# Performance work log

Hardware: AMD Instinct MI355X
Metric: run time of the kernel (lower is better)

The kernel has to match this reference:

```python
import jax, jax.numpy as jnp
import numpy as np

H, KVH, D, HID = 32, 8, 128, 4096
ROPE_LEN, THETA = 8192, 10000.0
MASK_OUT, MIN_REMAIN = 0.9, 128


def _rope_tables(dtype):
    inv_freq = 1.0 / (THETA ** (jnp.arange(0, D, 2, dtype=jnp.float32) / D))
    freqs = jnp.arange(ROPE_LEN, dtype=jnp.float32)[:, None] * inv_freq[None, :]
    emb = jnp.concatenate([freqs, freqs], axis=-1)  # [8192, 128]
    return jnp.cos(emb).astype(dtype), jnp.sin(emb).astype(dtype)


def _rotate_half(x):
    x1, x2 = x[..., : D // 2], x[..., D // 2:]
    return jnp.concatenate([-x2, x1], axis=-1)


def _apply_rope(x, pos, cos, sin):
    c, s = cos[pos][None, None], sin[pos][None, None]  # [1,1,L,D]
    return x * c + _rotate_half(x) * s


def setup_inputs() -> dict:
    key = jax.random.key(0)
    ks = jax.random.split(key, 11)
    S = 4096
    f = jnp.float32
    return {
        "hidden_states": jax.random.normal(ks[0], (1, 1, HID), f),
        "key_cache": jax.random.normal(ks[1], (1, H, S, D), f),
        "val_cache": jax.random.normal(ks[2], (1, H, S, D), f),
        "Wq": jax.random.normal(ks[3], (HID, HID), f) * 0.02,
        "Wk": jax.random.normal(ks[4], (HID, KVH * D), f) * 0.02,
        "Wv": jax.random.normal(ks[5], (HID, KVH * D), f) * 0.02,
        "Wo": jax.random.normal(ks[6], (HID, HID), f) * 0.02,
        "hash_proj1": jax.random.normal(ks[7], (1, H, D, D), f) * 0.001,
        "hash_bias1": jnp.zeros((1, H, 1, D), f),
        "hash_proj2": jax.random.normal(ks[8], (1, H, D, D), f) * 0.001,
        "hash_bias2": jnp.zeros((1, H, 1, D), f),
    }


def reference(hidden_states, key_cache, val_cache, Wq, Wk, Wv, Wo,
              hash_proj1, hash_bias1, hash_proj2, hash_bias2):
    B, Q, _ = hidden_states.shape  # B=1, Q=1 (decode step)
    G = H // KVH
    dtype = hidden_states.dtype

    # projections -> [B, heads, Q, D]
    ques = (hidden_states @ Wq).reshape(B, Q, H, D).transpose(0, 2, 1, 3)
    k_new = (hidden_states @ Wk).reshape(B, Q, KVH, D).transpose(0, 2, 1, 3)
    v_new = (hidden_states @ Wv).reshape(B, Q, KVH, D).transpose(0, 2, 1, 3)
    k_new = jnp.repeat(k_new, G, axis=1)  # repeat_kv
    v_new = jnp.repeat(v_new, G, axis=1)

    keys = jnp.concatenate([key_cache, k_new], axis=2)  # [1,H,K,D]
    vals = jnp.concatenate([val_cache, v_new], axis=2)
    K = keys.shape[2]

    cos, sin = _rope_tables(dtype)
    q_pos = K - Q + jnp.arange(Q)
    k_pos = jnp.arange(K)
    q_r = _apply_rope(ques, q_pos, cos, sin)
    k_r = _apply_rope(keys, k_pos, cos, sin)

    # per-head hash MLP: silu layer with residue, then linear layer with residue
    def hash_fn(x):
        h = jax.nn.silu(jnp.einsum('bhld,bhde->bhle', x, hash_proj1) + hash_bias1) + x
        h = (jnp.einsum('bhld,bhde->bhle', h, hash_proj2) + hash_bias2) + h
        return h

    q_hash = jnp.sign(hash_fn(q_r))
    k_hash = jnp.sign(hash_fn(k_r))
    draft_score = jnp.einsum('bhqd,bhkd->bhqk', q_hash, k_hash)  # LSH similarity

    num_remain = max(min(K, MIN_REMAIN), K - int(K * MASK_OUT))
    _, idx = jax.lax.top_k(draft_score, num_remain)  # [B,H,Q,num_remain]

    neg = jnp.finfo(dtype).min
    mask = jnp.full((B, H, Q, K), neg, dtype=dtype)
    bi = jnp.arange(B)[:, None, None, None]
    hi = jnp.arange(H)[None, :, None, None]
    qi = jnp.arange(Q)[None, None, :, None]
    mask = mask.at[bi, hi, qi, idx].set(0.0)

    scores = jnp.einsum('bhqd,bhkd->bhqk', q_r, k_r) / np.sqrt(D) + mask
    attn = jax.nn.softmax(scores, axis=-1)
    out = jnp.einsum('bhqk,bhkd->bhqd', attn, vals)
    out = out.transpose(0, 2, 1, 3).reshape(B, Q, HID) @ Wo
    return out
```

## Files before the change

### kernel.cpp

```cpp
#include <hip/hip_runtime.h>
#include <math.h>

#define NH 32
#define NKVH 8
#define HD 128

typedef _Float16 half8 __attribute__((ext_vector_type(8)));
typedef float f32x4 __attribute__((ext_vector_type(4)));

#define OFF_QPROJ 0
#define OFF_KNEW  4096
#define OFF_VNEW  5120
#define OFF_QR    6144
#define OFF_QHASH 10240
#define OFF_TAB   10368

__global__ void init_kernel(float* __restrict__ ws, float* __restrict__ out, int K) {
    int idx = blockIdx.x * 256 + threadIdx.x;
    if (idx < K * 64) {
        int pos = idx >> 6, d = idx & 63;
        double inv = exp(-((double)d / 64.0) * log(10000.0));
        double ang = (double)pos * inv;
        double s, c;
        sincos(ang, &s, &c);
        ws[OFF_TAB + idx]                  = (float)c;
        ws[OFF_TAB + (size_t)K * 64 + idx] = (float)s;
    }
    if (idx < 6144) ws[OFF_QPROJ + idx] = 0.f;
    if (idx < 4096) out[idx] = 0.f;
    size_t off_attn = OFF_TAB + 2 * (size_t)K * 64 + 2 * (size_t)NH * K;
    if (idx < 4096) ws[off_attn + idx] = 0.f;
}

__global__ __launch_bounds__(256) void pt16_prep(const float* __restrict__ hp1,
        const float* __restrict__ hp2, float* __restrict__ ws, int K) {
    const int tg  = blockIdx.x * 256 + threadIdx.x;
    const int h   = blockIdx.y >> 1, mat = blockIdx.y & 1;
    const int lane = tg & 63, nt = (tg >> 6) & 7, ks = tg >> 9;
    const int kbase = ks * 32 + ((tg >> 4) & 3) * 8;
    const int n = nt * 16 + (tg & 15);
    const float* P = (mat ? hp2 : hp1) + (size_t)h * 16384;
    half8 v;
#pragma unroll
    for (int j = 0; j < 8; ++j) v[j] = (_Float16)P[(size_t)(kbase + j) * 128 + n];
    size_t off_pt = OFF_TAB + 2 * (size_t)K * 64 + 2 * (size_t)NH * K + 4096 + 2 * (size_t)NH * 512;
    ((half8*)(ws + off_pt))[(size_t)(h * 2 + mat) * 2048 + tg] = v;
}

__global__ __launch_bounds__(256) void qkv_gemv(const float* __restrict__ hidden,
        const float* __restrict__ Wq, const float* __restrict__ Wk,
        const float* __restrict__ Wv, float* __restrict__ ws) {
    __shared__ float hs[32];
    const int tid = threadIdx.x;
    const int col = (blockIdx.x * 256 + tid) * 4;
    const int i0  = blockIdx.y * 32;
    if (tid < 32) hs[tid] = hidden[i0 + tid];
    __syncthreads();
    const float* W; int ld, wcol;
    if (col < 4096)      { W = Wq; ld = 4096; wcol = col; }
    else if (col < 5120) { W = Wk; ld = 1024; wcol = col - 4096; }
    else                 { W = Wv; ld = 1024; wcol = col - 5120; }
    const float* p = W + (size_t)i0 * ld + wcol;
    float4 acc = {0.f, 0.f, 0.f, 0.f};
#pragma unroll 4
    for (int ii = 0; ii < 32; ++ii) {
        float4 w4 = *(const float4*)p;
        float hh = hs[ii];
        acc.x = fmaf(hh, w4.x, acc.x); acc.y = fmaf(hh, w4.y, acc.y);
        acc.z = fmaf(hh, w4.z, acc.z); acc.w = fmaf(hh, w4.w, acc.w);
        p += ld;
    }
    atomicAdd(&ws[OFF_QPROJ + col + 0], acc.x);
    atomicAdd(&ws[OFF_QPROJ + col + 1], acc.y);
    atomicAdd(&ws[OFF_QPROJ + col + 2], acc.z);
    atomicAdd(&ws[OFF_QPROJ + col + 3], acc.w);
}

__global__ __launch_bounds__(128) void qhash_kernel(const float* __restrict__ hp1,
        const float* __restrict__ hb1, const float* __restrict__ hp2,
        const float* __restrict__ hb2, float* __restrict__ ws, int S) {
    const int h = blockIdx.x, d = threadIdx.x;
    const int K = S + 1;
    __shared__ float X[128], H1[128];
    float q  = ws[OFF_QPROJ + h * 128 + d];
    float qp = ws[OFF_QPROJ + h * 128 + (d ^ 64)];
    const float* cosT = ws + OFF_TAB;
    const float* sinT = cosT + (size_t)K * 64;
    float cs = cosT[(size_t)S * 64 + (d & 63)];
    float sn = sinT[(size_t)S * 64 + (d & 63)];
    float r = (d < 64) ? -qp : qp;
    float qr = q * cs + r * sn;
    X[d] = qr;
    ws[OFF_QR + h * 128 + d] = qr;
    __syncthreads();
    const float* P1 = hp1 + (size_t)h * 16384;
    float t = hb1[h * 128 + d];
    for (int i = 0; i < 128; ++i) t = fmaf(X[i], P1[i * 128 + d], t);
    float u = t / (1.f + expf(-t)) + X[d];
    H1[d] = u;
    __syncthreads();
    const float* P2 = hp2 + (size_t)h * 16384;
    float t2 = hb2[h * 128 + d] + u;
    for (int i = 0; i < 128; ++i) t2 = fmaf(H1[i], P2[i * 128 + d], t2);
    unsigned long long bal = __ballot(t2 > 0.f);
    if ((d & 63) == 0)
        ((unsigned long long*)(ws + OFF_QHASH))[h * 2 + (d >> 6)] = bal;
}

__global__ __launch_bounds__(256, 2) void key_kernel(const float* __restrict__ key_cache,
        const float* __restrict__ hb1, const float* __restrict__ hb2,
        float* __restrict__ ws, int S) {
    const int K  = S + 1;
    const int h  = blockIdx.y;
    const int k0 = blockIdx.x * 64;
    const int tid = threadIdx.x;
    const int wv = tid >> 6, lane = tid & 63;

    __shared__ float    XF[64 * 132];
    __shared__ _Float16 XH[64 * 136];
    __shared__ _Float16 BST[2 * 4096];
    __shared__ unsigned short HB[64 * 8];
    __shared__ float    QV[128];

    const float* cosT = ws + OFF_TAB;
    const float* sinT = cosT + (size_t)K * 64;
    float* scores = ws + OFF_TAB + 2 * (size_t)K * 64;
    int*   draft  = (int*)(scores + (size_t)NH * K);
    size_t off_pt = OFF_TAB + 2 * (size_t)K * 64 + 2 * (size_t)NH * K + 4096 + 2 * (size_t)NH * 512;
    const _Float16* PT1 = (const _Float16*)(ws + off_pt) + (size_t)(h * 2 + 0) * 16384;
    const _Float16* PT2 = (const _Float16*)(ws + off_pt) + (size_t)(h * 2 + 1) * 16384;

    if (tid < 128) QV[tid] = ws[OFF_QR + h * 128 + tid];

    const int key = tid >> 2, qq = tid & 3, d0 = qq * 16;
    const int kg = k0 + key;
    float lo[16], hi[16];
    if (kg < K) {
        const float* row = (kg < S) ? key_cache + ((size_t)h * S + kg) * 128
                                    : ws + OFF_KNEW + (h >> 2) * 128;
#pragma unroll
        for (int i4 = 0; i4 < 4; ++i4) {
            float4 xa = *(const float4*)(row + d0 + i4 * 4);
            float4 xb = *(const float4*)(row + 64 + d0 + i4 * 4);
            float4 cc = *(const float4*)(cosT + (size_t)kg * 64 + d0 + i4 * 4);
            float4 ss = *(const float4*)(sinT + (size_t)kg * 64 + d0 + i4 * 4);
            lo[i4*4+0] = xa.x * cc.x - xb.x * ss.x;  hi[i4*4+0] = xb.x * cc.x + xa.x * ss.x;
            lo[i4*4+1] = xa.y * cc.y - xb.y * ss.y;  hi[i4*4+1] = xb.y * cc.y + xa.y * ss.y;
            lo[i4*4+2] = xa.z * cc.z - xb.z * ss.z;  hi[i4*4+2] = xb.z * cc.z + xa.z * ss.z;
            lo[i4*4+3] = xa.w * cc.w - xb.w * ss.w;  hi[i4*4+3] = xb.w * cc.w + xa.w * ss.w;
        }
    } else {
#pragma unroll
        for (int i = 0; i < 16; ++i) { lo[i] = 0.f; hi[i] = 0.f; }
    }
#pragma unroll
    for (int i = 0; i < 16; ++i) {
        XF[key * 132 + d0 + i]      = lo[i];
        XF[key * 132 + 64 + d0 + i] = hi[i];
        XH[key * 136 + d0 + i]      = (_Float16)lo[i];
        XH[key * 136 + 64 + d0 + i] = (_Float16)hi[i];
    }
    __syncthreads();

    {
        float part = 0.f;
#pragma unroll
        for (int i = 0; i < 16; ++i)
            part = fmaf(QV[d0 + i], lo[i], fmaf(QV[64 + d0 + i], hi[i], part));
        part += __shfl_xor(part, 1);
        part += __shfl_xor(part, 2);
        if (qq == 0 && kg < K) scores[(size_t)h * K + kg] = part * 0.08838834764831845f;
    }

    float b1v[8], b2v[8];
#pragma unroll
    for (int nt = 0; nt < 8; ++nt) {
        b1v[nt] = hb1[h * 128 + nt * 16 + (lane & 15)];
        b2v[nt] = hb2[h * 128 + nt * 16 + (lane & 15)];
    }

    f32x4 acc[8];
    const int m = lane & 15, quad = lane >> 4;

#define GEMM_MFMA(PT)                                                              \
    {                                                                              \
        _Pragma("unroll") for (int nt = 0; nt < 8; ++nt)                           \
            acc[nt] = (f32x4){0.f, 0.f, 0.f, 0.f};                                 \
        const half8* src = (const half8*)(PT);                                     \
        half8 pre0 = src[tid * 2], pre1 = src[tid * 2 + 1];                        \
        for (int c = 0; c < 4; ++c) {                                              \
            half8* dst = (half8*)&BST[(c & 1) * 4096];                             \
            dst[tid * 2] = pre0; dst[tid * 2 + 1] = pre1;                          \
            __syncthreads();                                                       \
            if (c < 3) {                                                           \
                pre0 = src[(c + 1) * 512 + tid * 2];                               \
                pre1 = src[(c + 1) * 512 + tid * 2 + 1];                           \
            }                                                                      \
            half8 afrag = *(const half8*)&XH[(wv * 16 + m) * 136 + c * 32 + quad * 8]; \
            _Pragma("unroll") for (int nt = 0; nt < 8; ++nt) {                     \
                half8 bfrag = *(const half8*)&BST[(c & 1) * 4096 + nt * 512 + lane * 8]; \
                acc[nt] = __builtin_amdgcn_mfma_f32_16x16x32_f16(afrag, bfrag, acc[nt], 0, 0, 0); \
            }                                                                      \
        }                                                                          \
    }

    GEMM_MFMA(PT1)
#pragma unroll
    for (int nt = 0; nt < 8; ++nt) {
        const int n = nt * 16 + m;
#pragma unroll
        for (int r = 0; r < 4; ++r) {
            const int kk = wv * 16 + quad * 4 + r;
            float t = acc[nt][r] + b1v[nt];
            float x = XF[kk * 132 + n];
            float h1v = t / (1.f + expf(-t)) + x;
            XF[kk * 132 + n] = h1v;
            XH[kk * 136 + n] = (_Float16)h1v;
        }
    }

    GEMM_MFMA(PT2)
#pragma unroll
    for (int nt = 0; nt < 8; ++nt) {
        const int n = nt * 16 + m;
#pragma unroll
        for (int r = 0; r < 4; ++r) {
            const int kk = wv * 16 + quad * 4 + r;
            float t2 = acc[nt][r] + b2v[nt] + XF[kk * 132 + n];
            unsigned long long bal = __ballot(t2 > 0.f);
            if (m == 0) {
                unsigned short chunk = (unsigned short)((bal >> (quad * 16)) & 0xFFFFull);
                HB[(wv * 16 + quad * 4 + r) * 8 + nt] = chunk;
            }
        }
    }
    __syncthreads();

    if (tid < 64) {
        int kgd = k0 + tid;
        if (kgd < K) {
            const unsigned short* hbp = &HB[tid * 8];
            unsigned w0 = (unsigned)hbp[0] | ((unsigned)hbp[1] << 16);
            unsigned w1 = (unsigned)hbp[2] | ((unsigned)hbp[3] << 16);
            unsigned w2 = (unsigned)hbp[4] | ((unsigned)hbp[5] << 16);
            unsigned w3 = (unsigned)hbp[6] | ((unsigned)hbp[7] << 16);
            const unsigned* qh = (const unsigned*)(ws + OFF_QHASH) + h * 4;
            int ham = __popc(w0 ^ qh[0]) + __popc(w1 ^ qh[1])
                    + __popc(w2 ^ qh[2]) + __popc(w3 ^ qh[3]);
            draft[(size_t)h * K + kgd] = 128 - 2 * ham;
        }
    }
#undef GEMM_MFMA
}

__global__ __launch_bounds__(256) void select_kernel(float* __restrict__ ws, int S, int nrem) {
    const int K = S + 1;
    const int h = blockIdx.x;
    const int tid = threadIdx.x;
    __shared__ int hist[129];
    __shared__ int sel_idx[512];
    __shared__ float red[256];
    __shared__ int wtot[4];
    __shared__ int sh_tval, sh_r, sh_cnt, sh_run;

    float* scoresB = ws + OFF_TAB + 2 * (size_t)K * 64;
    const int* draft = (const int*)(scoresB + (size_t)NH * K) + (size_t)h * K;
    const float* sc = scoresB + (size_t)h * K;
    float* attn = scoresB + 2 * (size_t)NH * K;
    int*   selidx_g = (int*)(attn + 4096) + h * 512;
    float* selw_g   = (attn + 4096 + NH * 512) + h * 512;

    for (int i = tid; i < 129; i += 256) hist[i] = 0;
    if (tid == 0) { sh_cnt = 0; sh_run = 0; }
    __syncthreads();
    for (int k = tid; k < K; k += 256) atomicAdd(&hist[(draft[k] + 128) >> 1], 1);
    __syncthreads();
    if (tid == 0) {
        int cum = 0, tb = 0, r = nrem;
        for (int b = 128; b >= 0; --b) {
            int c = hist[b];
            if (cum + c >= nrem) { tb = b; r = nrem - cum; break; }
            cum += c;
        }
        sh_tval = tb * 2 - 128; sh_r = r;
    }
    __syncthreads();
    const int tval = sh_tval, r = sh_r;
    const int lane = tid & 63, wave = tid >> 6;
    for (int base = 0; base < K; base += 256) {
        int k = base + tid;
        bool valid = (k < K);
        int dv = valid ? draft[k] : -1000;
        bool eq = valid && (dv == tval);
        bool gt = valid && (dv > tval);
        unsigned long long bal = __ballot(eq);
        if (lane == 0) wtot[wave] = __popcll(bal);
        __syncthreads();
        int woff = 0;
        for (int w = 0; w < wave; ++w) woff += wtot[w];
        int rank = sh_run + woff + __popcll(bal & ((1ull << lane) - 1ull));
        bool sel = gt || (eq && (rank < r));
        if (sel) sel_idx[atomicAdd(&sh_cnt, 1)] = k;
        __syncthreads();
        if (tid == 0) sh_run += wtot[0] + wtot[1] + wtot[2] + wtot[3];
        __syncthreads();
    }
    float mmax = -3.402823466e38f;
    for (int li = tid; li < nrem; li += 256) mmax = fmaxf(mmax, sc[sel_idx[li]]);
    red[tid] = mmax; __syncthreads();
    for (int s2 = 128; s2 > 0; s2 >>= 1) {
        if (tid < s2) red[tid] = fmaxf(red[tid], red[tid + s2]);
        __syncthreads();
    }
    mmax = red[0]; __syncthreads();
    float z = 0.f;
    for (int li = tid; li < nrem; li += 256) z += expf(sc[sel_idx[li]] - mmax);
    red[tid] = z; __syncthreads();
    for (int s2 = 128; s2 > 0; s2 >>= 1) {
        if (tid < s2) red[tid] += red[tid + s2];
        __syncthreads();
    }
    float Z = red[0]; __syncthreads();
    for (int li = tid; li < nrem; li += 256) {
        int idx = sel_idx[li];
        selidx_g[li] = idx;
        selw_g[li] = expf(sc[idx] - mmax) / Z;
    }
}

__global__ __launch_bounds__(256) void gather_kernel(const float* __restrict__ val_cache,
        float* __restrict__ ws, int S, int nrem) {
    const int K = S + 1;
    const int h = blockIdx.x, g = blockIdx.y;
    const int tid = threadIdx.x;
    const int d = tid & 127, pr = tid >> 7;
    float* scoresB = ws + OFF_TAB + 2 * (size_t)K * 64;
    float* attn = scoresB + 2 * (size_t)NH * K;
    const int*   selidx_g = (const int*)(attn + 4096) + h * 512;
    const float* selw_g   = (attn + 4096 + NH * 512) + h * 512;
    float acc = 0.f;
    for (int li = g * 2 + pr; li < nrem; li += 16) {
        int idx = selidx_g[li];
        float w = selw_g[li];
        const float* vr = (idx < S) ? val_cache + ((size_t)h * S + idx) * 128
                                    : ws + OFF_VNEW + (h >> 2) * 128;
        acc = fmaf(w, vr[d], acc);
    }
    atomicAdd(&attn[h * 128 + d], acc);
}

__global__ __launch_bounds__(256) void out_gemv(const float* __restrict__ Wo,
        const float* __restrict__ ws, float* __restrict__ out, int K) {
    __shared__ float hs[32];
    const int tid = threadIdx.x;
    const int col = (blockIdx.x * 256 + tid) * 4;
    const int i0  = blockIdx.y * 32;
    const float* ao = ws + OFF_TAB + 2 * (size_t)K * 64 + 2 * (size_t)NH * K;
    if (tid < 32) hs[tid] = ao[i0 + tid];
    __syncthreads();
    const float* p = Wo + (size_t)i0 * 4096 + col;
    float4 acc = {0.f, 0.f, 0.f, 0.f};
#pragma unroll 4
    for (int ii = 0; ii < 32; ++ii) {
        float4 w4 = *(const float4*)p;
        float hh = hs[ii];
        acc.x = fmaf(hh, w4.x, acc.x); acc.y = fmaf(hh, w4.y, acc.y);
        acc.z = fmaf(hh, w4.z, acc.z); acc.w = fmaf(hh, w4.w, acc.w);
        p += 4096;
    }
    atomicAdd(&out[col + 0], acc.x);
    atomicAdd(&out[col + 1], acc.y);
    atomicAdd(&out[col + 2], acc.z);
    atomicAdd(&out[col + 3], acc.w);
}

extern "C" void kernel_launch(void* const* d_in, const int* in_sizes, int n_in,
                              void* d_out, int out_size, void* d_ws, size_t ws_size,
                              hipStream_t stream) {
    const float* hidden = (const float*)d_in[0];
    const float* key_cache = (const float*)d_in[1];
    const float* val_cache = (const float*)d_in[2];
    const float* Wq = (const float*)d_in[3];
    const float* Wk = (const float*)d_in[4];
    const float* Wv = (const float*)d_in[5];
    const float* Wo = (const float*)d_in[6];
    const float* hp1 = (const float*)d_in[7];
    const float* hb1 = (const float*)d_in[8];
    const float* hp2 = (const float*)d_in[9];
    const float* hb2 = (const float*)d_in[10];
    float* out = (float*)d_out;
    float* ws  = (float*)d_ws;

    const int S = in_sizes[1] / (NH * HD);
    const int K = S + 1;
    int mn = (K < 128) ? K : 128;
    int nrem = K - (int)((double)K * 0.9);
    if (nrem < mn) nrem = mn;

    init_kernel<<<(K * 64 + 255) / 256, 256, 0, stream>>>(ws, out, K);
    pt16_prep<<<dim3(8, 64), 256, 0, stream>>>(hp1, hp2, ws, K);
    qkv_gemv<<<dim3(6, 128), 256, 0, stream>>>(hidden, Wq, Wk, Wv, ws);
    qhash_kernel<<<NH, 128, 0, stream>>>(hp1, hb1, hp2, hb2, ws, S);
    key_kernel<<<dim3((K + 63) / 64, NH), 256, 0, stream>>>(key_cache, hb1, hb2, ws, S);
    select_kernel<<<NH, 256, 0, stream>>>(ws, S, nrem);
    gather_kernel<<<dim3(NH, 8), 256, 0, stream>>>(val_cache, ws, S, nrem);
    out_gemv<<<dim3(4, 128), 256, 0, stream>>>(Wo, ws, out, K);
}
```

Baseline: 377.3 us.

## Merge prep kernels, drop key-kernel LDS staging, compute Hamming in registers

Folds the fp16 hash-projection repack into the init kernel, which removes one launch. The key kernel no longer stages B fragments or the query vector through shared memory and reads them straight from global, and it raises launch bounds to 3 blocks per CU. It also computes the Hamming distance in registers from ballots, which removes a sync and the HB buffer. The GEMVs now process 64 rows per block with two accumulators, and the gather kernel uses float2 per-wave streams with more blocks. The risks are more global/L2 traffic for the B fragments and register pressure from the higher occupancy target.

```diff
diff --git a/kernel.cpp b/kernel.cpp
--- a/kernel.cpp
+++ b/kernel.cpp
@@ -15,65 +15,71 @@
 #define OFF_QHASH 10240
 #define OFF_TAB   10368
 
-__global__ void init_kernel(float* __restrict__ ws, float* __restrict__ out, int K) {
-    int idx = blockIdx.x * 256 + threadIdx.x;
-    if (idx < K * 64) {
-        int pos = idx >> 6, d = idx & 63;
-        double inv = exp(-((double)d / 64.0) * log(10000.0));
-        double ang = (double)pos * inv;
-        double s, c;
-        sincos(ang, &s, &c);
-        ws[OFF_TAB + idx]                  = (float)c;
-        ws[OFF_TAB + (size_t)K * 64 + idx] = (float)s;
-    }
-    if (idx < 6144) ws[OFF_QPROJ + idx] = 0.f;
-    if (idx < 4096) out[idx] = 0.f;
-    size_t off_attn = OFF_TAB + 2 * (size_t)K * 64 + 2 * (size_t)NH * K;
-    if (idx < 4096) ws[off_attn + idx] = 0.f;
-}
-
-__global__ __launch_bounds__(256) void pt16_prep(const float* __restrict__ hp1,
-        const float* __restrict__ hp2, float* __restrict__ ws, int K) {
-    const int tg  = blockIdx.x * 256 + threadIdx.x;
-    const int h   = blockIdx.y >> 1, mat = blockIdx.y & 1;
-    const int lane = tg & 63, nt = (tg >> 6) & 7, ks = tg >> 9;
-    const int kbase = ks * 32 + ((tg >> 4) & 3) * 8;
-    const int n = nt * 16 + (tg & 15);
-    const float* P = (mat ? hp2 : hp1) + (size_t)h * 16384;
-    half8 v;
-#pragma unroll
-    for (int j = 0; j < 8; ++j) v[j] = (_Float16)P[(size_t)(kbase + j) * 128 + n];
-    size_t off_pt = OFF_TAB + 2 * (size_t)K * 64 + 2 * (size_t)NH * K + 4096 + 2 * (size_t)NH * 512;
-    ((half8*)(ws + off_pt))[(size_t)(h * 2 + mat) * 2048 + tg] = v;
+__global__ void init_kernel(const float* __restrict__ hp1, const float* __restrict__ hp2,
+                            float* __restrict__ ws, float* __restrict__ out,
+                            int K, int nInit) {
+    const int tid = threadIdx.x;
+    if ((int)blockIdx.x < nInit) {
+        int idx = blockIdx.x * 256 + tid;
+        if (idx < K * 64) {
+            int pos = idx >> 6, d = idx & 63;
+            double inv = exp(-((double)d / 64.0) * log(10000.0));
+            double ang = (double)pos * inv;
+            double s, c;
+            sincos(ang, &s, &c);
+            ws[OFF_TAB + idx]                  = (float)c;
+            ws[OFF_TAB + (size_t)K * 64 + idx] = (float)s;
+        }
+        if (idx < 6144) ws[OFF_QPROJ + idx] = 0.f;
+        if (idx < 4096) out[idx] = 0.f;
+        size_t off_attn = OFF_TAB + 2 * (size_t)K * 64 + 2 * (size_t)NH * K;
+        if (idx < 4096) ws[off_attn + idx] = 0.f;
+    } else {
+        int id = blockIdx.x - nInit;
+        int h2 = id >> 3;
+        int tg = (id & 7) * 256 + tid;
+        const int lane = tg & 63, nt = (tg >> 6) & 7, ks = tg >> 9;
+        const int kbase = ks * 32 + ((tg >> 4) & 3) * 8;
+        const int n = nt * 16 + (tg & 15);
+        const float* P = ((h2 & 1) ? hp2 : hp1) + (size_t)(h2 >> 1) * 16384;
+        half8 v;
+#pragma unroll
+        for (int j = 0; j < 8; ++j) v[j] = (_Float16)P[(size_t)(kbase + j) * 128 + n];
+        size_t off_pt = OFF_TAB + 2 * (size_t)K * 64 + 2 * (size_t)NH * K + 4096 + 2 * (size_t)NH * 512;
+        ((half8*)(ws + off_pt))[(size_t)h2 * 2048 + tg] = v;
+    }
 }
 
 __global__ __launch_bounds__(256) void qkv_gemv(const float* __restrict__ hidden,
         const float* __restrict__ Wq, const float* __restrict__ Wk,
         const float* __restrict__ Wv, float* __restrict__ ws) {
-    __shared__ float hs[32];
+    __shared__ float hs[64];
     const int tid = threadIdx.x;
     const int col = (blockIdx.x * 256 + tid) * 4;
-    const int i0  = blockIdx.y * 32;
-    if (tid < 32) hs[tid] = hidden[i0 + tid];
+    const int i0  = blockIdx.y * 64;
+    if (tid < 64) hs[tid] = hidden[i0 + tid];
     __syncthreads();
     const float* W; int ld, wcol;
     if (col < 4096)      { W = Wq; ld = 4096; wcol = col; }
     else if (col < 5120) { W = Wk; ld = 1024; wcol = col - 4096; }
     else                 { W = Wv; ld = 1024; wcol = col - 5120; }
     const float* p = W + (size_t)i0 * ld + wcol;
-    float4 acc = {0.f, 0.f, 0.f, 0.f};
+    float4 a0 = {0.f,0.f,0.f,0.f}, a1 = {0.f,0.f,0.f,0.f};
 #pragma unroll 4
-    for (int ii = 0; ii < 32; ++ii) {
-        float4 w4 = *(const float4*)p;
-        float hh = hs[ii];
-        acc.x = fmaf(hh, w4.x, acc.x); acc.y = fmaf(hh, w4.y, acc.y);
-        acc.z = fmaf(hh, w4.z, acc.z); acc.w = fmaf(hh, w4.w, acc.w);
-        p += ld;
-    }
-    atomicAdd(&ws[OFF_QPROJ + col + 0], acc.x);
-    atomicAdd(&ws[OFF_QPROJ + col + 1], acc.y);
-    atomicAdd(&ws[OFF_QPROJ + col + 2], acc.z);
-    atomicAdd(&ws[OFF_QPROJ + col + 3], acc.w);
+    for (int ii = 0; ii < 64; ii += 2) {
+        float4 w0 = *(const float4*)p;
+        float4 w1 = *(const float4*)(p + ld);
+        float h0 = hs[ii], h1 = hs[ii + 1];
+        a0.x = fmaf(h0, w0.x, a0.x); a0.y = fmaf(h0, w0.y, a0.y);
+        a0.z = fmaf(h0, w0.z, a0.z); a0.w = fmaf(h0, w0.w, a0.w);
+        a1.x = fmaf(h1, w1.x, a1.x); a1.y = fmaf(h1, w1.y, a1.y);
+        a1.z = fmaf(h1, w1.z, a1.z); a1.w = fmaf(h1, w1.w, a1.w);
+        p += 2 * (size_t)ld;
+    }
+    atomicAdd(&ws[OFF_QPROJ + col + 0], a0.x + a1.x);
+    atomicAdd(&ws[OFF_QPROJ + col + 1], a0.y + a1.y);
+    atomicAdd(&ws[OFF_QPROJ + col + 2], a0.z + a1.z);
+    atomicAdd(&ws[OFF_QPROJ + col + 3], a0.w + a1.w);
 }
 
 __global__ __launch_bounds__(128) void qhash_kernel(const float* __restrict__ hp1,
@@ -107,7 +113,7 @@
         ((unsigned long long*)(ws + OFF_QHASH))[h * 2 + (d >> 6)] = bal;
 }
 
-__global__ __launch_bounds__(256, 2) void key_kernel(const float* __restrict__ key_cache,
+__global__ __launch_bounds__(256, 3) void key_kernel(const float* __restrict__ key_cache,
         const float* __restrict__ hb1, const float* __restrict__ hb2,
         float* __restrict__ ws, int S) {
     const int K  = S + 1;
@@ -115,22 +121,18 @@
     const int k0 = blockIdx.x * 64;
     const int tid = threadIdx.x;
     const int wv = tid >> 6, lane = tid & 63;
+    const int m = lane & 15, quad = lane >> 4;
 
     __shared__ float    XF[64 * 132];
     __shared__ _Float16 XH[64 * 136];
-    __shared__ _Float16 BST[2 * 4096];
-    __shared__ unsigned short HB[64 * 8];
-    __shared__ float    QV[128];
 
     const float* cosT = ws + OFF_TAB;
     const float* sinT = cosT + (size_t)K * 64;
     float* scores = ws + OFF_TAB + 2 * (size_t)K * 64;
     int*   draft  = (int*)(scores + (size_t)NH * K);
     size_t off_pt = OFF_TAB + 2 * (size_t)K * 64 + 2 * (size_t)NH * K + 4096 + 2 * (size_t)NH * 512;
-    const _Float16* PT1 = (const _Float16*)(ws + off_pt) + (size_t)(h * 2 + 0) * 16384;
-    const _Float16* PT2 = (const _Float16*)(ws + off_pt) + (size_t)(h * 2 + 1) * 16384;
-
-    if (tid < 128) QV[tid] = ws[OFF_QR + h * 128 + tid];
+    const half8* PT1 = (const half8*)((const _Float16*)(ws + off_pt) + (size_t)(h * 2) * 16384);
+    const half8* PT2 = PT1 + 2048;
 
     const int key = tid >> 2, qq = tid & 3, d0 = qq * 16;
     const int kg = k0 + key;
@@ -154,19 +156,37 @@
         for (int i = 0; i < 16; ++i) { lo[i] = 0.f; hi[i] = 0.f; }
     }
 #pragma unroll
-    for (int i = 0; i < 16; ++i) {
-        XF[key * 132 + d0 + i]      = lo[i];
-        XF[key * 132 + 64 + d0 + i] = hi[i];
-        XH[key * 136 + d0 + i]      = (_Float16)lo[i];
-        XH[key * 136 + 64 + d0 + i] = (_Float16)hi[i];
-    }
-    __syncthreads();
-
+    for (int i4 = 0; i4 < 4; ++i4) {
+        float4 l4 = {lo[i4*4], lo[i4*4+1], lo[i4*4+2], lo[i4*4+3]};
+        float4 h4 = {hi[i4*4], hi[i4*4+1], hi[i4*4+2], hi[i4*4+3]};
+        *(float4*)&XF[key * 132 + d0 + i4 * 4]      = l4;
+        *(float4*)&XF[key * 132 + 64 + d0 + i4 * 4] = h4;
+    }
     {
+        half8 hl0, hl1, hh0, hh1;
+#pragma unroll
+        for (int i = 0; i < 8; ++i) {
+            hl0[i] = (_Float16)lo[i];     hl1[i] = (_Float16)lo[8 + i];
+            hh0[i] = (_Float16)hi[i];     hh1[i] = (_Float16)hi[8 + i];
+        }
+        *(half8*)&XH[key * 136 + d0]          = hl0;
+        *(half8*)&XH[key * 136 + d0 + 8]      = hl1;
+        *(half8*)&XH[key * 136 + 64 + d0]     = hh0;
+        *(half8*)&XH[key * 136 + 64 + d0 + 8] = hh1;
+    }
+
+    {
+        const float* qr = ws + OFF_QR + h * 128;
         float part = 0.f;
 #pragma unroll
-        for (int i = 0; i < 16; ++i)
-            part = fmaf(QV[d0 + i], lo[i], fmaf(QV[64 + d0 + i], hi[i], part));
+        for (int i4 = 0; i4 < 4; ++i4) {
+            float4 qa = *(const float4*)(qr + d0 + i4 * 4);
+            float4 qb = *(const float4*)(qr + 64 + d0 + i4 * 4);
+            part = fmaf(qa.x, lo[i4*4+0], fmaf(qb.x, hi[i4*4+0], part));
+            part = fmaf(qa.y, lo[i4*4+1], fmaf(qb.y, hi[i4*4+1], part));
+            part = fmaf(qa.z, lo[i4*4+2], fmaf(qb.z, hi[i4*4+2], part));
+            part = fmaf(qa.w, lo[i4*4+3], fmaf(qb.w, hi[i4*4+3], part));
+        }
         part += __shfl_xor(part, 1);
         part += __shfl_xor(part, 2);
         if (qq == 0 && kg < K) scores[(size_t)h * K + kg] = part * 0.08838834764831845f;
@@ -175,30 +195,28 @@
     float b1v[8], b2v[8];
 #pragma unroll
     for (int nt = 0; nt < 8; ++nt) {
-        b1v[nt] = hb1[h * 128 + nt * 16 + (lane & 15)];
-        b2v[nt] = hb2[h * 128 + nt * 16 + (lane & 15)];
+        b1v[nt] = hb1[h * 128 + nt * 16 + m];
+        b2v[nt] = hb2[h * 128 + nt * 16 + m];
+    }
+    unsigned short qh16[8];
+    {
+        uint4 q4 = *(const uint4*)((const unsigned*)(ws + OFF_QHASH) + h * 4);
+        unsigned qa[4] = {q4.x, q4.y, q4.z, q4.w};
+#pragma unroll
+        for (int nt = 0; nt < 8; ++nt)
+            qh16[nt] = (unsigned short)((qa[nt >> 1] >> ((nt & 1) * 16)) & 0xFFFFu);
     }
 
     f32x4 acc[8];
-    const int m = lane & 15, quad = lane >> 4;
 
 #define GEMM_MFMA(PT)                                                              \
     {                                                                              \
         _Pragma("unroll") for (int nt = 0; nt < 8; ++nt)                           \
             acc[nt] = (f32x4){0.f, 0.f, 0.f, 0.f};                                 \
-        const half8* src = (const half8*)(PT);                                     \
-        half8 pre0 = src[tid * 2], pre1 = src[tid * 2 + 1];                        \
-        for (int c = 0; c < 4; ++c) {                                              \
-            half8* dst = (half8*)&BST[(c & 1) * 4096];                             \
-            dst[tid * 2] = pre0; dst[tid * 2 + 1] = pre1;                          \
-            __syncthreads();                                                       \
-            if (c < 3) {                                                           \
-                pre0 = src[(c + 1) * 512 + tid * 2];                               \
-                pre1 = src[(c + 1) * 512 + tid * 2 + 1];                           \
-            }                                                                      \
+        _Pragma("unroll") for (int c = 0; c < 4; ++c) {                            \
             half8 afrag = *(const half8*)&XH[(wv * 16 + m) * 136 + c * 32 + quad * 8]; \
             _Pragma("unroll") for (int nt = 0; nt < 8; ++nt) {                     \
-                half8 bfrag = *(const half8*)&BST[(c & 1) * 4096 + nt * 512 + lane * 8]; \
+                half8 bfrag = (PT)[c * 512 + nt * 64 + lane];                      \
                 acc[nt] = __builtin_amdgcn_mfma_f32_16x16x32_f16(afrag, bfrag, acc[nt], 0, 0, 0); \
             }                                                                      \
         }                                                                          \
@@ -220,34 +238,26 @@
     }
 
     GEMM_MFMA(PT2)
-#pragma unroll
-    for (int nt = 0; nt < 8; ++nt) {
-        const int n = nt * 16 + m;
-#pragma unroll
-        for (int r = 0; r < 4; ++r) {
-            const int kk = wv * 16 + quad * 4 + r;
-            float t2 = acc[nt][r] + b2v[nt] + XF[kk * 132 + n];
-            unsigned long long bal = __ballot(t2 > 0.f);
-            if (m == 0) {
-                unsigned short chunk = (unsigned short)((bal >> (quad * 16)) & 0xFFFFull);
-                HB[(wv * 16 + quad * 4 + r) * 8 + nt] = chunk;
+    {
+        int ham[4] = {0, 0, 0, 0};
+#pragma unroll
+        for (int nt = 0; nt < 8; ++nt) {
+            const int n = nt * 16 + m;
+#pragma unroll
+            for (int r = 0; r < 4; ++r) {
+                const int kk = wv * 16 + quad * 4 + r;
+                float t2 = acc[nt][r] + b2v[nt] + XF[kk * 132 + n];
+                unsigned long long bal = __ballot(t2 > 0.f);
+                unsigned bits = (unsigned)(bal >> (quad * 16)) & 0xFFFFu;
+                ham[r] += __popc(bits ^ (unsigned)qh16[nt]);
             }
         }
-    }
-    __syncthreads();
-
-    if (tid < 64) {
-        int kgd = k0 + tid;
-        if (kgd < K) {
-            const unsigned short* hbp = &HB[tid * 8];
-            unsigned w0 = (unsigned)hbp[0] | ((unsigned)hbp[1] << 16);
-            unsigned w1 = (unsigned)hbp[2] | ((unsigned)hbp[3] << 16);
-            unsigned w2 = (unsigned)hbp[4] | ((unsigned)hbp[5] << 16);
-            unsigned w3 = (unsigned)hbp[6] | ((unsigned)hbp[7] << 16);
-            const unsigned* qh = (const unsigned*)(ws + OFF_QHASH) + h * 4;
-            int ham = __popc(w0 ^ qh[0]) + __popc(w1 ^ qh[1])
-                    + __popc(w2 ^ qh[2]) + __popc(w3 ^ qh[3]);
-            draft[(size_t)h * K + kgd] = 128 - 2 * ham;
+        if (m == 0) {
+#pragma unroll
+            for (int r = 0; r < 4; ++r) {
+                int kgd = k0 + wv * 16 + quad * 4 + r;
+                if (kgd < K) draft[(size_t)h * K + kgd] = 128 - 2 * ham[r];
+            }
         }
     }
 #undef GEMM_MFMA
@@ -333,45 +343,52 @@
     const int K = S + 1;
     const int h = blockIdx.x, g = blockIdx.y;
     const int tid = threadIdx.x;
-    const int d = tid & 127, pr = tid >> 7;
+    const int wave = tid >> 6, lane = tid & 63;
+    const int stream = g * 4 + wave;
     float* scoresB = ws + OFF_TAB + 2 * (size_t)K * 64;
     float* attn = scoresB + 2 * (size_t)NH * K;
     const int*   selidx_g = (const int*)(attn + 4096) + h * 512;
     const float* selw_g   = (attn + 4096 + NH * 512) + h * 512;
-    float acc = 0.f;
-    for (int li = g * 2 + pr; li < nrem; li += 16) {
+    float ax = 0.f, ay = 0.f;
+    for (int li = stream; li < nrem; li += 64) {
         int idx = selidx_g[li];
         float w = selw_g[li];
         const float* vr = (idx < S) ? val_cache + ((size_t)h * S + idx) * 128
                                     : ws + OFF_VNEW + (h >> 2) * 128;
-        acc = fmaf(w, vr[d], acc);
-    }
-    atomicAdd(&attn[h * 128 + d], acc);
+        float2 v = ((const float2*)vr)[lane];
+        ax = fmaf(w, v.x, ax);
+        ay = fmaf(w, v.y, ay);
+    }
+    atomicAdd(&attn[h * 128 + lane * 2 + 0], ax);
+    atomicAdd(&attn[h * 128 + lane * 2 + 1], ay);
 }
 
 __global__ __launch_bounds__(256) void out_gemv(const float* __restrict__ Wo,
         const float* __restrict__ ws, float* __restrict__ out, int K) {
-    __shared__ float hs[32];
+    __shared__ float hs[64];
     const int tid = threadIdx.x;
     const int col = (blockIdx.x * 256 + tid) * 4;
-    const int i0  = blockIdx.y * 32;
+    const int i0  = blockIdx.y * 64;
     const float* ao = ws + OFF_TAB + 2 * (size_t)K * 64 + 2 * (size_t)NH * K;
-    if (tid < 32) hs[tid] = ao[i0 + tid];
+    if (tid < 64) hs[tid] = ao[i0 + tid];
     __syncthreads();
     const float* p = Wo + (size_t)i0 * 4096 + col;
-    float4 acc = {0.f, 0.f, 0.f, 0.f};
+    float4 a0 = {0.f,0.f,0.f,0.f}, a1 = {0.f,0.f,0.f,0.f};
 #pragma unroll 4
-    for (int ii = 0; ii < 32; ++ii) {
-        float4 w4 = *(const float4*)p;
-        float hh = hs[ii];
-        acc.x = fmaf(hh, w4.x, acc.x); acc.y = fmaf(hh, w4.y, acc.y);
-        acc.z = fmaf(hh, w4.z, acc.z); acc.w = fmaf(hh, w4.w, acc.w);
-        p += 4096;
-    }
-    atomicAdd(&out[col + 0], acc.x);
-    atomicAdd(&out[col + 1], acc.y);
-    atomicAdd(&out[col + 2], acc.z);
-    atomicAdd(&out[col + 3], acc.w);
+    for (int ii = 0; ii < 64; ii += 2) {
+        float4 w0 = *(const float4*)p;
+        float4 w1 = *(const float4*)(p + 4096);
+        float h0 = hs[ii], h1 = hs[ii + 1];
+        a0.x = fmaf(h0, w0.x, a0.x); a0.y = fmaf(h0, w0.y, a0.y);
+        a0.z = fmaf(h0, w0.z, a0.z); a0.w = fmaf(h0, w0.w, a0.w);
+        a1.x = fmaf(h1, w1.x, a1.x); a1.y = fmaf(h1, w1.y, a1.y);
+        a1.z = fmaf(h1, w1.z, a1.z); a1.w = fmaf(h1, w1.w, a1.w);
+        p += 8192;
+    }
+    atomicAdd(&out[col + 0], a0.x + a1.x);
+    atomicAdd(&out[col + 1], a0.y + a1.y);
+    atomicAdd(&out[col + 2], a0.z + a1.z);
+    atomicAdd(&out[col + 3], a0.w + a1.w);
 }
 
 extern "C" void kernel_launch(void* const* d_in, const int* in_sizes, int n_in,
@@ -397,12 +414,12 @@
     int nrem = K - (int)((double)K * 0.9);
     if (nrem < mn) nrem = mn;
 
-    init_kernel<<<(K * 64 + 255) / 256, 256, 0, stream>>>(ws, out, K);
-    pt16_prep<<<dim3(8, 64), 256, 0, stream>>>(hp1, hp2, ws, K);
-    qkv_gemv<<<dim3(6, 128), 256, 0, stream>>>(hidden, Wq, Wk, Wv, ws);
+    const int nInit = (K * 64 + 255) / 256;
+    init_kernel<<<nInit + 512, 256, 0, stream>>>(hp1, hp2, ws, out, K, nInit);
+    qkv_gemv<<<dim3(6, 64), 256, 0, stream>>>(hidden, Wq, Wk, Wv, ws);
     qhash_kernel<<<NH, 128, 0, stream>>>(hp1, hb1, hp2, hb2, ws, S);
     key_kernel<<<dim3((K + 63) / 64, NH), 256, 0, stream>>>(key_cache, hb1, hb2, ws, S);
     select_kernel<<<NH, 256, 0, stream>>>(ws, S, nrem);
-    gather_kernel<<<dim3(NH, 8), 256, 0, stream>>>(val_cache, ws, S, nrem);
-    out_gemv<<<dim3(4, 128), 256, 0, stream>>>(Wo, ws, out, K);
-}
+    gather_kernel<<<dim3(NH, 16), 256, 0, stream>>>(val_cache, ws, S, nrem);
+    out_gemv<<<dim3(4, 64), 256, 0, stream>>>(Wo, ws, out, K);
+}
```

After: 346.5 us. -8.2%, faster.
